# Kernel tuning notes

Hardware: AMD Instinct MI355X
Metric: run time of the kernel (lower is better)

## Reference

```python
import jax, jax.numpy as jnp
import numpy as np

B, S, E = 2, 2048, 2048
H, KV, D = 16, 4, 128
G = H // KV
ROPE_THETA = 10000.0


def setup_inputs() -> dict:
    key = jax.random.key(0)
    ks = jax.random.split(key, 8)
    std = 0.02
    return {
        "x": jax.random.normal(ks[0], (B, S, E), jnp.float32),
        "Wq": jax.random.normal(ks[1], (H * D, E), jnp.float32) * std,
        "bq": jax.random.normal(ks[2], (H * D,), jnp.float32) * std,
        "Wk": jax.random.normal(ks[3], (KV * D, E), jnp.float32) * std,
        "bk": jax.random.normal(ks[4], (KV * D,), jnp.float32) * std,
        "Wv": jax.random.normal(ks[5], (KV * D, E), jnp.float32) * std,
        "bv": jax.random.normal(ks[6], (KV * D,), jnp.float32) * std,
        "Wo": jax.random.normal(ks[7], (E, H * D), jnp.float32) * std,
    }


def _rope_cos_sin(seq_len, head_dim):
    inv_freq = 1.0 / (ROPE_THETA ** (jnp.arange(0, head_dim, 2, dtype=jnp.float32) / head_dim))
    pos = jnp.arange(seq_len, dtype=jnp.float32)  # rope scale factor = 1.0
    freqs = pos[:, None] * inv_freq[None, :]        # [S, D/2]
    emb = jnp.concatenate([freqs, freqs], axis=-1)  # [S, D]
    return jnp.cos(emb), jnp.sin(emb)


def _apply_rope(t, cos, sin):
    # t: [..., S, <extra dims>, D]; cos/sin: [S, D] broadcast over extra dims
    half = t.shape[-1] // 2
    extra = t.ndim - 3  # dims between S (axis 1) and D (last)
    c = cos.reshape((1, cos.shape[0]) + (1,) * extra + (cos.shape[1],))
    s = sin.reshape((1, sin.shape[0]) + (1,) * extra + (sin.shape[1],))
    rot = jnp.concatenate([-t[..., half:], t[..., :half]], axis=-1)
    return t * c + rot * s


def reference(x, Wq, bq, Wk, bk, Wv, bv, Wo):
    b, s, e = x.shape
    # QKV projections (biases on q/k/v, none on o)
    q = (jnp.einsum("bse,he->bsh", x, Wq) + bq).reshape(b, s, KV, G, D)
    k = (jnp.einsum("bse,he->bsh", x, Wk) + bk).reshape(b, s, KV, D)
    v = (jnp.einsum("bse,he->bsh", x, Wv) + bv).reshape(b, s, KV, D)

    cos, sin = _rope_cos_sin(s, D)
    q = _apply_rope(q, cos, sin)
    k = _apply_rope(k, cos, sin)

    scale = 1.0 / jnp.sqrt(jnp.float32(D))
    # GQA: q heads grouped per kv head; k/v broadcast over group dim
    scores = jnp.einsum("bskgd,btkd->bkgst", q, k) * scale  # [B,KV,G,S,S]
    causal = jnp.tril(jnp.ones((s, s), dtype=bool))
    scores = jnp.where(causal, scores, jnp.float32(-1e9))
    attn = jax.nn.softmax(scores, axis=-1)
    out = jnp.einsum("bkgst,btkd->bskgd", attn, v).reshape(b, s, H * D)
    return jnp.einsum("bsh,eh->bse", out, Wo)
```

## Files before the change

### kernel.cpp

```cpp
#include <hip/hip_runtime.h>
#include <hip/hip_bf16.h>
#include <math.h>

#define BB 2
#define SS 2048
#define EE 2048
#define HH 16
#define KVH 4
#define DD 128

typedef short short8 __attribute__((ext_vector_type(8)));
typedef float f32x4 __attribute__((ext_vector_type(4)));

__device__ __forceinline__ unsigned int f2bf1(float x) {
    union { float f; unsigned int u; } v; v.f = x;
    return (v.u + 0x7FFFu + ((v.u >> 16) & 1u)) >> 16;
}
__device__ __forceinline__ unsigned int packbf(float a, float b) {
    return f2bf1(a) | (f2bf1(b) << 16);
}
__device__ __forceinline__ void gl_lds16(const void* g, void* l) {
    __builtin_amdgcn_global_load_lds(
        (const __attribute__((address_space(1))) unsigned int*)g,
        (__attribute__((address_space(3))) unsigned int*)l,
        16, 0, 0);
}

#define DPPF(x, ctrl) __int_as_float(__builtin_amdgcn_update_dpp( \
    0, __float_as_int(x), ctrl, 0xf, 0xf, true))
__device__ __forceinline__ float rmax16(float x) {
    x = fmaxf(x, DPPF(x, 0xB1));
    x = fmaxf(x, DPPF(x, 0x4E));
    x = fmaxf(x, DPPF(x, 0x141));
    x = fmaxf(x, DPPF(x, 0x140));
    return x;
}
__device__ __forceinline__ float rsum16(float x) {
    x += DPPF(x, 0xB1);
    x += DPPF(x, 0x4E);
    x += DPPF(x, 0x141);
    x += DPPF(x, 0x140);
    return x;
}

__global__ __launch_bounds__(256) void cvt_all_kernel(
    const float* __restrict__ x,  const float* __restrict__ Wq,
    const float* __restrict__ Wk, const float* __restrict__ Wv,
    const float* __restrict__ Wo, const float* __restrict__ bq,
    const float* __restrict__ bk, const float* __restrict__ bv,
    unsigned short* __restrict__ xb, unsigned short* __restrict__ wqkv,
    unsigned short* __restrict__ wob, float* __restrict__ bqkv)
{
    long id = (long)blockIdx.x * 256 + threadIdx.x;
    const float* src; unsigned short* dst; long j;
    if (id < 2097152)      { j = id;           src = x;  dst = xb; }
    else if (id < 3145728) { j = id - 2097152; src = Wq; dst = wqkv; }
    else if (id < 3407872) { j = id - 3145728; src = Wk; dst = wqkv + 4194304; }
    else if (id < 3670016) { j = id - 3407872; src = Wv; dst = wqkv + 5242880; }
    else if (id < 4718592) { j = id - 3670016; src = Wo; dst = wob; }
    else if (id < 4719360) {
        long c = (id - 4718592) * 4;
#pragma unroll
        for (int e = 0; e < 4; ++e) {
            long cc = c + e;
            bqkv[cc] = (cc < 2048) ? bq[cc] : (cc < 2560 ? bk[cc - 2048] : bv[cc - 2560]);
        }
        return;
    } else return;
    float4 f = ((const float4*)src)[j];
    ((uint2*)dst)[j] = make_uint2(packbf(f.x, f.y), packbf(f.z, f.w));
}

template <bool OUT_BF16>
__global__ __launch_bounds__(256) void gemm_mfma_kernel(
    const unsigned short* __restrict__ A, const unsigned short* __restrict__ W,
    const float* __restrict__ bias, void* __restrict__ Cout,
    int M, int N, int K)
{
    __shared__ unsigned short As[128 * 32];
    __shared__ unsigned short Bs[128 * 32];

    const int tid  = threadIdx.x;
    const int w    = tid >> 6;
    const int lane = tid & 63;
    const int quad = lane >> 4;
    const int l16  = lane & 15;
    const int wr   = w >> 1, wc = w & 1;
    const int m0 = blockIdx.y * 128, n0 = blockIdx.x * 128;

    f32x4 acc[4][4];
#pragma unroll
    for (int i = 0; i < 4; ++i)
#pragma unroll
        for (int j = 0; j < 4; ++j) acc[i][j] = (f32x4){0.f, 0.f, 0.f, 0.f};

    const unsigned short* Ag = A + (size_t)(m0 + w * 32 + (lane >> 2)) * K + (lane & 3) * 8;
    const unsigned short* Wg = W + (size_t)(n0 + w * 32 + (lane >> 2)) * K + (lane & 3) * 8;
    unsigned short* AsB = &As[(w * 32) * 32];
    unsigned short* BsB = &Bs[(w * 32) * 32];

    for (int k0 = 0; k0 < K; k0 += 32) {
        gl_lds16(Ag + k0, AsB);
        gl_lds16(Ag + k0 + (size_t)16 * K, AsB + 16 * 32);
        gl_lds16(Wg + k0, BsB);
        gl_lds16(Wg + k0 + (size_t)16 * K, BsB + 16 * 32);
        __syncthreads();

        short8 a_f[4], b_f[4];
#pragma unroll
        for (int i = 0; i < 4; ++i)
            a_f[i] = *(const short8*)&As[(wr * 64 + i * 16 + l16) * 32 + quad * 8];
#pragma unroll
        for (int j = 0; j < 4; ++j)
            b_f[j] = *(const short8*)&Bs[(wc * 64 + j * 16 + l16) * 32 + quad * 8];
#pragma unroll
        for (int i = 0; i < 4; ++i)
#pragma unroll
            for (int j = 0; j < 4; ++j)
                acc[i][j] = __builtin_amdgcn_mfma_f32_16x16x32_bf16(a_f[i], b_f[j], acc[i][j], 0, 0, 0);
        __syncthreads();
    }

    float bj[4];
#pragma unroll
    for (int j = 0; j < 4; ++j)
        bj[j] = bias ? bias[n0 + wc * 64 + j * 16 + l16] : 0.0f;
#pragma unroll
    for (int i = 0; i < 4; ++i) {
#pragma unroll
        for (int r = 0; r < 4; ++r) {
            size_t row = m0 + wr * 64 + i * 16 + quad * 4 + r;
#pragma unroll
            for (int j = 0; j < 4; ++j) {
                size_t col = n0 + wc * 64 + j * 16 + l16;
                float val = acc[i][j][r] + bj[j];
                if (OUT_BF16)
                    ((unsigned short*)Cout)[row * N + col] = (unsigned short)f2bf1(val);
                else
                    ((float*)Cout)[row * N + col] = val;
            }
        }
    }
}

__global__ __launch_bounds__(64) void rope_kernel(unsigned short* __restrict__ qkv)
{
    int bix = blockIdx.x;
    int m, col;
    if (bix < 65536) { m = bix >> 4; col = (bix & 15) * 128; }
    else { int i = bix - 65536; m = i >> 2; col = 2048 + (i & 3) * 128; }
    int s = m & (SS - 1);
    int d = threadIdx.x;
    unsigned short* p = qkv + (size_t)m * 3072 + col;
    float inv_freq = expf(-(float)d * (logf(10000.0f) / 64.0f));
    float fr = (float)s * inv_freq;
    float c = cosf(fr), sn = sinf(fr);
    union { unsigned int u; float f; } x1, x2;
    x1.u = ((unsigned int)p[d]) << 16;
    x2.u = ((unsigned int)p[d + 64]) << 16;
    p[d]      = (unsigned short)f2bf1(x1.f * c - x2.f * sn);
    p[d + 64] = (unsigned short)f2bf1(x2.f * c + x1.f * sn);
}

__global__ __launch_bounds__(256, 2) void attn_mfma_kernel(
    const unsigned short* __restrict__ qkv, unsigned short* __restrict__ o)
{
    __shared__ unsigned int Ks_u[64 * 64];
    __shared__ unsigned int Vs_u[128 * 32];
    __shared__ unsigned short Ps[4][32 * 64];

    const int tid  = threadIdx.x;
    const int w    = tid >> 6;
    const int lane = tid & 63;
    const int quad = lane >> 4;
    const int l16  = lane & 15;
    const int qt   = 15 - blockIdx.x;
    const int h    = blockIdx.y;
    const int b    = blockIdx.z;
    const int kv   = h >> 2;

    const float k2 = 0.12752789744920764f;
    const int q0 = qt * 128;
    const int nt = 2 * qt + 2;

    const unsigned short* kbase = qkv + (size_t)b * SS * 3072 + 2048 + kv * 128;
    const unsigned short* vbase = kbase + 512;

    const int kc  = tid & 15;
    const int kp0 = tid >> 4;
    const int vpp = tid >> 3;
    const int vd0 = (tid & 7) * 16;

    short8 qf[2][4];
#pragma unroll
    for (int s = 0; s < 2; ++s) {
        const unsigned short* qp =
            qkv + (size_t)(b * SS + q0 + w * 32 + s * 16 + l16) * 3072 + h * 128 + quad * 8;
#pragma unroll
        for (int ks = 0; ks < 4; ++ks)
            qf[s][ks] = *(const short8*)(qp + ks * 32);
    }

    uint4 kpre[4], vpa[2], vpb[2];
    {
        const unsigned short* kg = kbase + (size_t)kp0 * 3072 + kc * 8;
#pragma unroll
        for (int rr = 0; rr < 4; ++rr)
            kpre[rr] = *(const uint4*)(kg + (size_t)rr * 16 * 3072);
        const unsigned short* vg = vbase + (size_t)(2 * vpp) * 3072 + vd0;
        vpa[0] = *(const uint4*)(vg);
        vpa[1] = *(const uint4*)(vg + 8);
        vpb[0] = *(const uint4*)(vg + 3072);
        vpb[1] = *(const uint4*)(vg + 3072 + 8);
    }

    float m_r[2][4], l_r[2][4];
    f32x4 Oacc[2][8];
#pragma unroll
    for (int s = 0; s < 2; ++s)
#pragma unroll
        for (int r = 0; r < 4; ++r) { m_r[s][r] = -1e30f; l_r[s][r] = 0.0f; }
#pragma unroll
    for (int s = 0; s < 2; ++s)
#pragma unroll
        for (int ot = 0; ot < 8; ++ot) Oacc[s][ot] = (f32x4){0.f, 0.f, 0.f, 0.f};

    for (int t = 0; t < nt; ++t) {
        if (t) __syncthreads();

#pragma unroll
        for (int rr = 0; rr < 4; ++rr) {
            int pos = kp0 + rr * 16;
            int key = (kp0 + rr) & 7;
            *(uint4*)&Ks_u[pos * 64 + (kc ^ key) * 4] = kpre[rr];
        }
        {
            const unsigned int* pa = (const unsigned int*)vpa;
            const unsigned int* pb = (const unsigned int*)vpb;
#pragma unroll
            for (int j = 0; j < 8; ++j) {
                unsigned lo = __builtin_amdgcn_perm(pb[j], pa[j], 0x05040100);
                unsigned hi = __builtin_amdgcn_perm(pb[j], pa[j], 0x07060302);
                int d0 = vd0 + 2 * j;
                int g  = d0 >> 4;
                int k0 = (d0 + g) & 7;
                int k1 = (d0 + 1 + g) & 7;
                Vs_u[d0 * 32 + (((vpp >> 2) ^ k0) & 7) * 4 + (vpp & 3)] = lo;
                Vs_u[(d0 + 1) * 32 + (((vpp >> 2) ^ k1) & 7) * 4 + (vpp & 3)] = hi;
            }
        }
        __syncthreads();

        if (t + 1 < nt) {
            const unsigned short* kg = kbase + (size_t)((t + 1) * 64 + kp0) * 3072 + kc * 8;
#pragma unroll
            for (int rr = 0; rr < 4; ++rr)
                kpre[rr] = *(const uint4*)(kg + (size_t)rr * 16 * 3072);
            const unsigned short* vg = vbase + (size_t)((t + 1) * 64 + 2 * vpp) * 3072 + vd0;
            vpa[0] = *(const uint4*)(vg);
            vpa[1] = *(const uint4*)(vg + 8);
            vpb[0] = *(const uint4*)(vg + 3072);
            vpb[1] = *(const uint4*)(vg + 3072 + 8);
        }

        f32x4 S0[4], S1[4];
#pragma unroll
        for (int ct = 0; ct < 4; ++ct) {
            f32x4 s0 = (f32x4){0.f, 0.f, 0.f, 0.f};
            f32x4 s1 = (f32x4){0.f, 0.f, 0.f, 0.f};
            const int row = ct * 16 + l16;
            const int key = (l16 + ct) & 7;
#pragma unroll
            for (int ks = 0; ks < 4; ++ks) {
                short8 kf = *(const short8*)&Ks_u[row * 64 + ((ks * 4 + quad) ^ key) * 4];
                s0 = __builtin_amdgcn_mfma_f32_16x16x32_bf16(qf[0][ks], kf, s0, 0, 0, 0);
                s1 = __builtin_amdgcn_mfma_f32_16x16x32_bf16(qf[1][ks], kf, s1, 0, 0, 0);
            }
            S0[ct] = s0; S1[ct] = s1;
        }

        if (t >= nt - 2) {
            const int p0 = t * 64;
            const int rw = q0 + w * 32 + quad * 4;
#pragma unroll
            for (int ct = 0; ct < 4; ++ct) {
                const int col = p0 + ct * 16 + l16;
#pragma unroll
                for (int r = 0; r < 4; ++r) {
                    if (col > rw + r)      S0[ct][r] = -1e30f;
                    if (col > rw + 16 + r) S1[ct][r] = -1e30f;
                }
            }
        }

#pragma unroll
        for (int s = 0; s < 2; ++s) {
            f32x4* S = s ? S1 : S0;
#pragma unroll
            for (int r = 0; r < 4; ++r) {
                float c0 = fmaxf(fmaxf(S[0][r], S[1][r]), fmaxf(S[2][r], S[3][r]));
                c0 = rmax16(c0);
                float mnew = fmaxf(m_r[s][r], c0);
                float alpha = exp2f((m_r[s][r] - mnew) * k2);
                m_r[s][r] = mnew;
                float mh = mnew * k2;
                float rs = 0.0f;
                const int prow = s * 16 + quad * 4 + r;
                const int pkey = prow & 7;
#pragma unroll
                for (int ct = 0; ct < 4; ++ct) {
                    float p = exp2f(S[ct][r] * k2 - mh);
                    rs += p;
                    int chunk = ct * 2 + (l16 >> 3);
                    union { float f; unsigned u; } pu; pu.f = p;
                    Ps[w][prow * 64 + (chunk ^ pkey) * 8 + (l16 & 7)] =
                        (unsigned short)((pu.u + 0x8000u) >> 16);
                }
                rs = rsum16(rs);
                l_r[s][r] = l_r[s][r] * alpha + rs;
#pragma unroll
                for (int ot = 0; ot < 8; ++ot) Oacc[s][ot][r] *= alpha;
            }
        }

        {
            const int pk = l16 & 7;
            short8 pf00 = *(const short8*)&Ps[w][(l16)      * 64 + ((quad)     ^ pk) * 8];
            short8 pf01 = *(const short8*)&Ps[w][(l16)      * 64 + ((4 + quad) ^ pk) * 8];
            short8 pf10 = *(const short8*)&Ps[w][(16 + l16) * 64 + ((quad)     ^ pk) * 8];
            short8 pf11 = *(const short8*)&Ps[w][(16 + l16) * 64 + ((4 + quad) ^ pk) * 8];
#pragma unroll
            for (int ot = 0; ot < 8; ++ot) {
                const int d = ot * 16 + l16;
                const int vkey = (l16 + ot) & 7;
                short8 v0 = *(const short8*)&Vs_u[d * 32 + ((quad) ^ vkey) * 4];
                Oacc[0][ot] = __builtin_amdgcn_mfma_f32_16x16x32_bf16(pf00, v0, Oacc[0][ot], 0, 0, 0);
                Oacc[1][ot] = __builtin_amdgcn_mfma_f32_16x16x32_bf16(pf10, v0, Oacc[1][ot], 0, 0, 0);
                short8 v1 = *(const short8*)&Vs_u[d * 32 + ((4 + quad) ^ vkey) * 4];
                Oacc[0][ot] = __builtin_amdgcn_mfma_f32_16x16x32_bf16(pf01, v1, Oacc[0][ot], 0, 0, 0);
                Oacc[1][ot] = __builtin_amdgcn_mfma_f32_16x16x32_bf16(pf11, v1, Oacc[1][ot], 0, 0, 0);
            }
        }
    }

#pragma unroll
    for (int s = 0; s < 2; ++s) {
        float inv[4];
#pragma unroll
        for (int r = 0; r < 4; ++r) inv[r] = 1.0f / l_r[s][r];
#pragma unroll
        for (int r = 0; r < 4; ++r) {
            const int row = quad * 4 + r;
#pragma unroll
            for (int ot = 0; ot < 8; ot += 2) {
                unsigned pv = packbf(Oacc[s][ot][r] * inv[r], 0.0f) |
                              (packbf(Oacc[s][ot + 1][r] * inv[r], 0.0f) << 16);
                Ps[w][row * 128 + ot * 16 + l16]       = (unsigned short)(pv & 0xffffu);
                Ps[w][row * 128 + (ot + 1) * 16 + l16] = (unsigned short)(pv >> 16);
            }
        }
#pragma unroll
        for (int i = 0; i < 4; ++i) {
            const int row = i * 4 + quad;
            uint4 val = *(const uint4*)&Ps[w][row * 128 + l16 * 8];
            unsigned short* op =
                o + (size_t)(b * SS + q0 + w * 32 + s * 16 + row) * 2048 + h * 128 + l16 * 8;
            *(uint4*)op = val;
        }
        if (s == 0) __builtin_amdgcn_s_waitcnt(0);
    }
}

extern "C" void kernel_launch(void* const* d_in, const int* in_sizes, int n_in,
                              void* d_out, int out_size, void* d_ws, size_t ws_size,
                              hipStream_t stream)
{
    const float* x  = (const float*)d_in[0];
    const float* Wq = (const float*)d_in[1];
    const float* bq = (const float*)d_in[2];
    const float* Wk = (const float*)d_in[3];
    const float* bk = (const float*)d_in[4];
    const float* Wv = (const float*)d_in[5];
    const float* bv = (const float*)d_in[6];
    const float* Wo = (const float*)d_in[7];
    float* out = (float*)d_out;

    const int M = BB * SS;
    char* wsb = (char*)d_ws;
    unsigned short* xb   = (unsigned short*)wsb;  wsb += (size_t)M * EE * 2;
    unsigned short* wqkv = (unsigned short*)wsb;  wsb += (size_t)3072 * EE * 2;
    unsigned short* wob  = (unsigned short*)wsb;  wsb += (size_t)EE * EE * 2;
    unsigned short* qkvb = (unsigned short*)wsb;  wsb += (size_t)M * 3072 * 2;
    unsigned short* abb  = (unsigned short*)wsb;  wsb += (size_t)M * 2048 * 2;
    float* bqkv = (float*)wsb;

    cvt_all_kernel<<<18435, 256, 0, stream>>>(x, Wq, Wk, Wv, Wo, bq, bk, bv,
                                              xb, wqkv, wob, bqkv);

    gemm_mfma_kernel<true><<<dim3(3072 / 128, M / 128), 256, 0, stream>>>(
        xb, wqkv, bqkv, qkvb, M, 3072, EE);

    rope_kernel<<<M * HH + M * KVH, 64, 0, stream>>>(qkvb);

    attn_mfma_kernel<<<dim3(16, HH, BB), 256, 0, stream>>>(qkvb, abb);

    gemm_mfma_kernel<false><<<dim3(EE / 128, M / 128), 256, 0, stream>>>(
        abb, wob, nullptr, out, M, EE, 2048);
}
```

Baseline: 425.0 us.

## Split KV range across two warp groups and pair causal query tiles per block

The attention kernel now runs 512 threads as two 256-thread groups. Each group processes alternating 64-key tiles for the same 128 query rows, and the two partial softmax states (m, l, O) are merged through shared memory at the end. Each block also handles two query tiles (jp and 15-jp), which balances causal work across blocks while halving the grid. The aim is more parallelism per block and an even load. The cost is double the LDS for K/V buffers, an extra cross-group merge with syncs, and fewer blocks overall.

```diff
diff --git a/kernel.cpp b/kernel.cpp
--- a/kernel.cpp
+++ b/kernel.cpp
@@ -162,212 +162,244 @@
     p[d + 64] = (unsigned short)f2bf1(x2.f * c + x1.f * sn);
 }
 
-__global__ __launch_bounds__(256, 2) void attn_mfma_kernel(
+__global__ __launch_bounds__(512, 2) void attn_mfma_kernel(
     const unsigned short* __restrict__ qkv, unsigned short* __restrict__ o)
 {
-    __shared__ unsigned int Ks_u[64 * 64];
-    __shared__ unsigned int Vs_u[128 * 32];
-    __shared__ unsigned short Ps[4][32 * 64];
+    __shared__ unsigned int Ks_u[2][64 * 64];
+    __shared__ unsigned int Vs_u[2][128 * 32];
+    __shared__ unsigned short Ps[8][32 * 64];
+    __shared__ float Ml[2][128][2];
 
     const int tid  = threadIdx.x;
-    const int w    = tid >> 6;
+    const int g    = tid >> 8;
+    const int tloc = tid & 255;
+    const int w8   = tid >> 6;
+    const int wg   = w8 & 3;
     const int lane = tid & 63;
     const int quad = lane >> 4;
     const int l16  = lane & 15;
-    const int qt   = 15 - blockIdx.x;
+    const int jp   = blockIdx.x;
     const int h    = blockIdx.y;
     const int b    = blockIdx.z;
     const int kv   = h >> 2;
 
     const float k2 = 0.12752789744920764f;
-    const int q0 = qt * 128;
-    const int nt = 2 * qt + 2;
 
     const unsigned short* kbase = qkv + (size_t)b * SS * 3072 + 2048 + kv * 128;
     const unsigned short* vbase = kbase + 512;
-
-    const int kc  = tid & 15;
-    const int kp0 = tid >> 4;
-    const int vpp = tid >> 3;
-    const int vd0 = (tid & 7) * 16;
-
-    short8 qf[2][4];
-#pragma unroll
-    for (int s = 0; s < 2; ++s) {
-        const unsigned short* qp =
-            qkv + (size_t)(b * SS + q0 + w * 32 + s * 16 + l16) * 3072 + h * 128 + quad * 8;
-#pragma unroll
-        for (int ks = 0; ks < 4; ++ks)
-            qf[s][ks] = *(const short8*)(qp + ks * 32);
-    }
-
-    uint4 kpre[4], vpa[2], vpb[2];
-    {
-        const unsigned short* kg = kbase + (size_t)kp0 * 3072 + kc * 8;
-#pragma unroll
-        for (int rr = 0; rr < 4; ++rr)
-            kpre[rr] = *(const uint4*)(kg + (size_t)rr * 16 * 3072);
-        const unsigned short* vg = vbase + (size_t)(2 * vpp) * 3072 + vd0;
-        vpa[0] = *(const uint4*)(vg);
-        vpa[1] = *(const uint4*)(vg + 8);
-        vpb[0] = *(const uint4*)(vg + 3072);
-        vpb[1] = *(const uint4*)(vg + 3072 + 8);
-    }
-
-    float m_r[2][4], l_r[2][4];
-    f32x4 Oacc[2][8];
-#pragma unroll
-    for (int s = 0; s < 2; ++s)
-#pragma unroll
-        for (int r = 0; r < 4; ++r) { m_r[s][r] = -1e30f; l_r[s][r] = 0.0f; }
-#pragma unroll
-    for (int s = 0; s < 2; ++s)
-#pragma unroll
-        for (int ot = 0; ot < 8; ++ot) Oacc[s][ot] = (f32x4){0.f, 0.f, 0.f, 0.f};
-
-    for (int t = 0; t < nt; ++t) {
-        if (t) __syncthreads();
-
-#pragma unroll
-        for (int rr = 0; rr < 4; ++rr) {
-            int pos = kp0 + rr * 16;
-            int key = (kp0 + rr) & 7;
-            *(uint4*)&Ks_u[pos * 64 + (kc ^ key) * 4] = kpre[rr];
-        }
+    unsigned int* Kg = Ks_u[g];
+    unsigned int* Vg = Vs_u[g];
+
+    const int kc  = tloc & 15;
+    const int kp0 = tloc >> 4;
+    const int vpp = tloc >> 3;
+    const int vd0 = (tloc & 7) * 16;
+
+    for (int pass = 0; pass < 2; ++pass) {
+        const int qt = pass ? (15 - jp) : jp;
+        const int q0 = qt * 128;
+        const int nt = qt + 1;
+
+        short8 qf[2][4];
+#pragma unroll
+        for (int s = 0; s < 2; ++s) {
+            const unsigned short* qp =
+                qkv + (size_t)(b * SS + q0 + wg * 32 + s * 16 + l16) * 3072 + h * 128 + quad * 8;
+#pragma unroll
+            for (int ks = 0; ks < 4; ++ks)
+                qf[s][ks] = *(const short8*)(qp + ks * 32);
+        }
+
+        uint4 kpre[4], vpa[2], vpb[2];
         {
-            const unsigned int* pa = (const unsigned int*)vpa;
-            const unsigned int* pb = (const unsigned int*)vpb;
-#pragma unroll
-            for (int j = 0; j < 8; ++j) {
-                unsigned lo = __builtin_amdgcn_perm(pb[j], pa[j], 0x05040100);
-                unsigned hi = __builtin_amdgcn_perm(pb[j], pa[j], 0x07060302);
-                int d0 = vd0 + 2 * j;
-                int g  = d0 >> 4;
-                int k0 = (d0 + g) & 7;
-                int k1 = (d0 + 1 + g) & 7;
-                Vs_u[d0 * 32 + (((vpp >> 2) ^ k0) & 7) * 4 + (vpp & 3)] = lo;
-                Vs_u[(d0 + 1) * 32 + (((vpp >> 2) ^ k1) & 7) * 4 + (vpp & 3)] = hi;
-            }
-        }
-        __syncthreads();
-
-        if (t + 1 < nt) {
-            const unsigned short* kg = kbase + (size_t)((t + 1) * 64 + kp0) * 3072 + kc * 8;
+            const unsigned short* kg2 = kbase + (size_t)(g * 64 + kp0) * 3072 + kc * 8;
 #pragma unroll
             for (int rr = 0; rr < 4; ++rr)
-                kpre[rr] = *(const uint4*)(kg + (size_t)rr * 16 * 3072);
-            const unsigned short* vg = vbase + (size_t)((t + 1) * 64 + 2 * vpp) * 3072 + vd0;
+                kpre[rr] = *(const uint4*)(kg2 + (size_t)rr * 16 * 3072);
+            const unsigned short* vg = vbase + (size_t)(g * 64 + 2 * vpp) * 3072 + vd0;
             vpa[0] = *(const uint4*)(vg);
             vpa[1] = *(const uint4*)(vg + 8);
             vpb[0] = *(const uint4*)(vg + 3072);
             vpb[1] = *(const uint4*)(vg + 3072 + 8);
         }
 
-        f32x4 S0[4], S1[4];
-#pragma unroll
-        for (int ct = 0; ct < 4; ++ct) {
-            f32x4 s0 = (f32x4){0.f, 0.f, 0.f, 0.f};
-            f32x4 s1 = (f32x4){0.f, 0.f, 0.f, 0.f};
-            const int row = ct * 16 + l16;
-            const int key = (l16 + ct) & 7;
-#pragma unroll
-            for (int ks = 0; ks < 4; ++ks) {
-                short8 kf = *(const short8*)&Ks_u[row * 64 + ((ks * 4 + quad) ^ key) * 4];
-                s0 = __builtin_amdgcn_mfma_f32_16x16x32_bf16(qf[0][ks], kf, s0, 0, 0, 0);
-                s1 = __builtin_amdgcn_mfma_f32_16x16x32_bf16(qf[1][ks], kf, s1, 0, 0, 0);
-            }
-            S0[ct] = s0; S1[ct] = s1;
-        }
-
-        if (t >= nt - 2) {
-            const int p0 = t * 64;
-            const int rw = q0 + w * 32 + quad * 4;
+        float m_r[2][4], l_r[2][4];
+        f32x4 Oacc[2][8];
+#pragma unroll
+        for (int s = 0; s < 2; ++s)
+#pragma unroll
+            for (int r = 0; r < 4; ++r) { m_r[s][r] = -1e30f; l_r[s][r] = 0.0f; }
+#pragma unroll
+        for (int s = 0; s < 2; ++s)
+#pragma unroll
+            for (int ot = 0; ot < 8; ++ot) Oacc[s][ot] = (f32x4){0.f, 0.f, 0.f, 0.f};
+
+        for (int t = 0; t < nt; ++t) {
+            __syncthreads();
+
+#pragma unroll
+            for (int rr = 0; rr < 4; ++rr) {
+                int pos = kp0 + rr * 16;
+                int key = (kp0 + rr) & 7;
+                *(uint4*)&Kg[pos * 64 + (kc ^ key) * 4] = kpre[rr];
+            }
+            {
+                const unsigned int* pa = (const unsigned int*)vpa;
+                const unsigned int* pb = (const unsigned int*)vpb;
+#pragma unroll
+                for (int j = 0; j < 8; ++j) {
+                    unsigned lo = __builtin_amdgcn_perm(pb[j], pa[j], 0x05040100);
+                    unsigned hi = __builtin_amdgcn_perm(pb[j], pa[j], 0x07060302);
+                    int d0 = vd0 + 2 * j;
+                    int gg = d0 >> 4;
+                    int k0 = (d0 + gg) & 7;
+                    int k1 = (d0 + 1 + gg) & 7;
+                    Vg[d0 * 32 + (((vpp >> 2) ^ k0) & 7) * 4 + (vpp & 3)] = lo;
+                    Vg[(d0 + 1) * 32 + (((vpp >> 2) ^ k1) & 7) * 4 + (vpp & 3)] = hi;
+                }
+            }
+            __syncthreads();
+
+            if (t + 1 < nt) {
+                const unsigned short* kg2 =
+                    kbase + (size_t)((t + 1) * 128 + g * 64 + kp0) * 3072 + kc * 8;
+#pragma unroll
+                for (int rr = 0; rr < 4; ++rr)
+                    kpre[rr] = *(const uint4*)(kg2 + (size_t)rr * 16 * 3072);
+                const unsigned short* vg =
+                    vbase + (size_t)((t + 1) * 128 + g * 64 + 2 * vpp) * 3072 + vd0;
+                vpa[0] = *(const uint4*)(vg);
+                vpa[1] = *(const uint4*)(vg + 8);
+                vpb[0] = *(const uint4*)(vg + 3072);
+                vpb[1] = *(const uint4*)(vg + 3072 + 8);
+            }
+
+            f32x4 S0[4], S1[4];
 #pragma unroll
             for (int ct = 0; ct < 4; ++ct) {
-                const int col = p0 + ct * 16 + l16;
+                f32x4 s0 = (f32x4){0.f, 0.f, 0.f, 0.f};
+                f32x4 s1 = (f32x4){0.f, 0.f, 0.f, 0.f};
+                const int row = ct * 16 + l16;
+                const int key = (l16 + ct) & 7;
+#pragma unroll
+                for (int ks = 0; ks < 4; ++ks) {
+                    short8 kf = *(const short8*)&Kg[row * 64 + ((ks * 4 + quad) ^ key) * 4];
+                    s0 = __builtin_amdgcn_mfma_f32_16x16x32_bf16(qf[0][ks], kf, s0, 0, 0, 0);
+                    s1 = __builtin_amdgcn_mfma_f32_16x16x32_bf16(qf[1][ks], kf, s1, 0, 0, 0);
+                }
+                S0[ct] = s0; S1[ct] = s1;
+            }
+
+            if (t == nt - 1) {
+                const int rw = q0 + wg * 32 + quad * 4;
+#pragma unroll
+                for (int ct = 0; ct < 4; ++ct) {
+                    const int col = t * 128 + g * 64 + ct * 16 + l16;
+#pragma unroll
+                    for (int r = 0; r < 4; ++r) {
+                        if (col > rw + r)      S0[ct][r] = -1e30f;
+                        if (col > rw + 16 + r) S1[ct][r] = -1e30f;
+                    }
+                }
+            }
+
+#pragma unroll
+            for (int s = 0; s < 2; ++s) {
+                f32x4* S = s ? S1 : S0;
 #pragma unroll
                 for (int r = 0; r < 4; ++r) {
-                    if (col > rw + r)      S0[ct][r] = -1e30f;
-                    if (col > rw + 16 + r) S1[ct][r] = -1e30f;
-                }
-            }
-        }
-
-#pragma unroll
-        for (int s = 0; s < 2; ++s) {
-            f32x4* S = s ? S1 : S0;
-#pragma unroll
-            for (int r = 0; r < 4; ++r) {
-                float c0 = fmaxf(fmaxf(S[0][r], S[1][r]), fmaxf(S[2][r], S[3][r]));
-                c0 = rmax16(c0);
-                float mnew = fmaxf(m_r[s][r], c0);
-                float alpha = exp2f((m_r[s][r] - mnew) * k2);
-                m_r[s][r] = mnew;
-                float mh = mnew * k2;
-                float rs = 0.0f;
-                const int prow = s * 16 + quad * 4 + r;
-                const int pkey = prow & 7;
-#pragma unroll
-                for (int ct = 0; ct < 4; ++ct) {
-                    float p = exp2f(S[ct][r] * k2 - mh);
-                    rs += p;
-                    int chunk = ct * 2 + (l16 >> 3);
-                    union { float f; unsigned u; } pu; pu.f = p;
-                    Ps[w][prow * 64 + (chunk ^ pkey) * 8 + (l16 & 7)] =
-                        (unsigned short)((pu.u + 0x8000u) >> 16);
-                }
-                rs = rsum16(rs);
-                l_r[s][r] = l_r[s][r] * alpha + rs;
-#pragma unroll
-                for (int ot = 0; ot < 8; ++ot) Oacc[s][ot][r] *= alpha;
-            }
-        }
-
+                    float c0 = fmaxf(fmaxf(S[0][r], S[1][r]), fmaxf(S[2][r], S[3][r]));
+                    c0 = rmax16(c0);
+                    float mnew = fmaxf(m_r[s][r], c0);
+                    float alpha = exp2f((m_r[s][r] - mnew) * k2);
+                    m_r[s][r] = mnew;
+                    float mh = mnew * k2;
+                    float rs = 0.0f;
+                    const int prow = s * 16 + quad * 4 + r;
+                    const int pkey = prow & 7;
+#pragma unroll
+                    for (int ct = 0; ct < 4; ++ct) {
+                        float p = exp2f(S[ct][r] * k2 - mh);
+                        rs += p;
+                        int chunk = ct * 2 + (l16 >> 3);
+                        union { float f; unsigned u; } pu; pu.f = p;
+                        Ps[w8][prow * 64 + (chunk ^ pkey) * 8 + (l16 & 7)] =
+                            (unsigned short)((pu.u + 0x8000u) >> 16);
+                    }
+                    rs = rsum16(rs);
+                    l_r[s][r] = l_r[s][r] * alpha + rs;
+#pragma unroll
+                    for (int ot = 0; ot < 8; ++ot) Oacc[s][ot][r] *= alpha;
+                }
+            }
+
+            {
+                const int pk = l16 & 7;
+                short8 pf00 = *(const short8*)&Ps[w8][(l16)      * 64 + ((quad)     ^ pk) * 8];
+                short8 pf01 = *(const short8*)&Ps[w8][(l16)      * 64 + ((4 + quad) ^ pk) * 8];
+                short8 pf10 = *(const short8*)&Ps[w8][(16 + l16) * 64 + ((quad)     ^ pk) * 8];
+                short8 pf11 = *(const short8*)&Ps[w8][(16 + l16) * 64 + ((4 + quad) ^ pk) * 8];
+#pragma unroll
+                for (int ot = 0; ot < 8; ++ot) {
+                    const int d = ot * 16 + l16;
+                    const int vkey = (l16 + ot) & 7;
+                    short8 v0 = *(const short8*)&Vg[d * 32 + ((quad) ^ vkey) * 4];
+                    Oacc[0][ot] = __builtin_amdgcn_mfma_f32_16x16x32_bf16(pf00, v0, Oacc[0][ot], 0, 0, 0);
+                    Oacc[1][ot] = __builtin_amdgcn_mfma_f32_16x16x32_bf16(pf10, v0, Oacc[1][ot], 0, 0, 0);
+                    short8 v1 = *(const short8*)&Vg[d * 32 + ((4 + quad) ^ vkey) * 4];
+                    Oacc[0][ot] = __builtin_amdgcn_mfma_f32_16x16x32_bf16(pf01, v1, Oacc[0][ot], 0, 0, 0);
+                    Oacc[1][ot] = __builtin_amdgcn_mfma_f32_16x16x32_bf16(pf11, v1, Oacc[1][ot], 0, 0, 0);
+                }
+            }
+        }
+
+        __syncthreads();
         {
-            const int pk = l16 & 7;
-            short8 pf00 = *(const short8*)&Ps[w][(l16)      * 64 + ((quad)     ^ pk) * 8];
-            short8 pf01 = *(const short8*)&Ps[w][(l16)      * 64 + ((4 + quad) ^ pk) * 8];
-            short8 pf10 = *(const short8*)&Ps[w][(16 + l16) * 64 + ((quad)     ^ pk) * 8];
-            short8 pf11 = *(const short8*)&Ps[w][(16 + l16) * 64 + ((4 + quad) ^ pk) * 8];
-#pragma unroll
-            for (int ot = 0; ot < 8; ++ot) {
-                const int d = ot * 16 + l16;
-                const int vkey = (l16 + ot) & 7;
-                short8 v0 = *(const short8*)&Vs_u[d * 32 + ((quad) ^ vkey) * 4];
-                Oacc[0][ot] = __builtin_amdgcn_mfma_f32_16x16x32_bf16(pf00, v0, Oacc[0][ot], 0, 0, 0);
-                Oacc[1][ot] = __builtin_amdgcn_mfma_f32_16x16x32_bf16(pf10, v0, Oacc[1][ot], 0, 0, 0);
-                short8 v1 = *(const short8*)&Vs_u[d * 32 + ((4 + quad) ^ vkey) * 4];
-                Oacc[0][ot] = __builtin_amdgcn_mfma_f32_16x16x32_bf16(pf01, v1, Oacc[0][ot], 0, 0, 0);
-                Oacc[1][ot] = __builtin_amdgcn_mfma_f32_16x16x32_bf16(pf11, v1, Oacc[1][ot], 0, 0, 0);
-            }
-        }
-    }
-
-#pragma unroll
-    for (int s = 0; s < 2; ++s) {
-        float inv[4];
-#pragma unroll
-        for (int r = 0; r < 4; ++r) inv[r] = 1.0f / l_r[s][r];
-#pragma unroll
-        for (int r = 0; r < 4; ++r) {
-            const int row = quad * 4 + r;
-#pragma unroll
-            for (int ot = 0; ot < 8; ot += 2) {
-                unsigned pv = packbf(Oacc[s][ot][r] * inv[r], 0.0f) |
-                              (packbf(Oacc[s][ot + 1][r] * inv[r], 0.0f) << 16);
-                Ps[w][row * 128 + ot * 16 + l16]       = (unsigned short)(pv & 0xffffu);
-                Ps[w][row * 128 + (ot + 1) * 16 + l16] = (unsigned short)(pv >> 16);
-            }
-        }
-#pragma unroll
-        for (int i = 0; i < 4; ++i) {
-            const int row = i * 4 + quad;
-            uint4 val = *(const uint4*)&Ps[w][row * 128 + l16 * 8];
-            unsigned short* op =
-                o + (size_t)(b * SS + q0 + w * 32 + s * 16 + row) * 2048 + h * 128 + l16 * 8;
-            *(uint4*)op = val;
-        }
-        if (s == 0) __builtin_amdgcn_s_waitcnt(0);
+            float* Ox = g ? (float*)Vs_u : (float*)Ks_u;
+            const int otb = (1 - g) * 4;
+#pragma unroll
+            for (int s = 0; s < 2; ++s) {
+                const int row = wg * 32 + s * 16 + quad * 4;
+#pragma unroll
+                for (int r = 0; r < 4; ++r) {
+#pragma unroll
+                    for (int oo = 0; oo < 4; ++oo)
+                        Ox[(row + r) * 64 + oo * 16 + l16] = Oacc[s][otb + oo][r];
+                    if (l16 == 0) {
+                        Ml[g][row + r][0] = m_r[s][r];
+                        Ml[g][row + r][1] = l_r[s][r];
+                    }
+                }
+            }
+        }
+        __syncthreads();
+        {
+            const float* Oi = g ? (const float*)Ks_u : (const float*)Vs_u;
+            const int go = 1 - g;
+            const int otb = g * 4;
+#pragma unroll
+            for (int s = 0; s < 2; ++s) {
+                const int row0 = wg * 32 + s * 16 + quad * 4;
+#pragma unroll
+                for (int r = 0; r < 4; ++r) {
+                    const int row = row0 + r;
+                    float mo = Ml[go][row][0];
+                    float lo2 = Ml[go][row][1];
+                    float mm = fmaxf(m_r[s][r], mo);
+                    float cw = exp2f((m_r[s][r] - mm) * k2);
+                    float co = exp2f((mo - mm) * k2);
+                    float inv = 1.0f / (l_r[s][r] * cw + lo2 * co);
+                    unsigned short* ob =
+                        o + (size_t)(b * SS + q0 + row) * 2048 + h * 128 + g * 64 + l16;
+#pragma unroll
+                    for (int oo = 0; oo < 4; ++oo) {
+                        float val = (Oacc[s][otb + oo][r] * cw +
+                                     Oi[row * 64 + oo * 16 + l16] * co) * inv;
+                        ob[oo * 16] = (unsigned short)f2bf1(val);
+                    }
+                }
+            }
+        }
     }
 }
 
@@ -402,7 +434,7 @@
 
     rope_kernel<<<M * HH + M * KVH, 64, 0, stream>>>(qkvb);
 
-    attn_mfma_kernel<<<dim3(16, HH, BB), 256, 0, stream>>>(qkvb, abb);
+    attn_mfma_kernel<<<dim3(8, HH, BB), 512, 0, stream>>>(qkvb, abb);
 
     gemm_mfma_kernel<false><<<dim3(EE / 128, M / 128), 256, 0, stream>>>(
         abb, wob, nullptr, out, M, EE, 2048);
```

Result: slower. 445.2 us (+4.7%).
